# Optimization experiments

Measured on AMD Instinct MI355X. Metric: run time of the kernel, lower is better.

## Reference

```python
import jax, jax.numpy as jnp
import numpy as np

TOP_K = 2

def setup_inputs() -> dict:
    key = jax.random.key(0)
    k1, k2, k3, k4 = jax.random.split(key, 4)
    N, D, E = 16384, 2048, 8
    inputs = jax.random.normal(k1, (N, D), dtype=jnp.float32)
    gate_w = jax.random.normal(k2, (D, E), dtype=jnp.float32) * 0.02
    expert_w = jax.random.normal(k3, (E, D, D), dtype=jnp.float32) * 0.02
    expert_b = jax.random.normal(k4, (E, D), dtype=jnp.float32) * 0.02
    return {"inputs": inputs, "gate_w": gate_w, "expert_w": expert_w, "expert_b": expert_b}

def reference(inputs, gate_w, expert_w, expert_b):
    # gate_logits: [N, E]
    gate_logits = inputs @ gate_w
    # top-k routing: weights/selected_experts are [N, k]
    topk_vals, topk_idx = jax.lax.top_k(gate_logits, TOP_K)
    # softmax over the k selected logits (fp32, matching F.softmax(..., dtype=float))
    weights = jax.nn.softmax(topk_vals.astype(jnp.float32), axis=1).astype(inputs.dtype)
    E = expert_w.shape[0]
    # combine_weights[n, e] = sum_k weights[n, k] * [topk_idx[n, k] == e]
    one_hot = jax.nn.one_hot(topk_idx, E, dtype=weights.dtype)  # [N, k, E]
    combine = jnp.einsum('nk,nke->ne', weights, one_hot)        # [N, E]
    # dense per-expert compute, masked by combine weights (same math as
    # the gather-matmul-scatter loop: unselected experts get weight 0)
    expert_out = jnp.einsum('nd,edh->neh', inputs, expert_w) + expert_b[None]  # [N, E, D]
    return jnp.einsum('ne,ned->nd', combine, expert_out)
```

## Files before the change

kernel.cpp:

```cpp
#include <hip/hip_runtime.h>
#include <stdint.h>

#define N_TOK 16384
#define DIM   2048
#define NEXP  8

#define NTILES 136
#define NSLOTS 36864

typedef __bf16 bf16x8 __attribute__((ext_vector_type(8)));
typedef float  f32x4  __attribute__((ext_vector_type(4)));

__device__ __forceinline__ unsigned short f2bf(float f) {
    union { float f; uint32_t u; } v; v.f = f;
    uint32_t u = v.u;
    u += 0x7fffu + ((u >> 16) & 1u);
    return (unsigned short)(u >> 16);
}

__global__ __launch_bounds__(256) void wconv_kernel(
    const float* __restrict__ W, unsigned short* __restrict__ Wt)
{
    __shared__ float tile[64][65];
    int e  = blockIdx.z;
    int kt = blockIdx.y * 64, nt = blockIdx.x * 64;
    int r4 = threadIdx.x >> 4;
    int c4 = threadIdx.x & 15;
    const float* src = W + ((size_t)e * DIM + kt) * DIM + nt;
#pragma unroll
    for (int i = 0; i < 4; ++i) {
        int r = i * 16 + r4;
        float4 v = *(const float4*)(src + (size_t)r * DIM + c4 * 4);
        tile[r][c4 * 4 + 0] = v.x; tile[r][c4 * 4 + 1] = v.y;
        tile[r][c4 * 4 + 2] = v.z; tile[r][c4 * 4 + 3] = v.w;
    }
    __syncthreads();
    unsigned short* dst = Wt + ((size_t)e * DIM + nt) * DIM + kt;
#pragma unroll
    for (int i = 0; i < 4; ++i) {
        int n = i * 16 + r4;
        ushort4 h;
        h.x = f2bf(tile[c4 * 4 + 0][n]);
        h.y = f2bf(tile[c4 * 4 + 1][n]);
        h.z = f2bf(tile[c4 * 4 + 2][n]);
        h.w = f2bf(tile[c4 * 4 + 3][n]);
        *(ushort4*)(dst + (size_t)n * DIM + c4 * 4) = h;
    }
}

__global__ __launch_bounds__(256) void gate_kernel(
    const float* __restrict__ X, const float* __restrict__ GW,
    unsigned short* __restrict__ Abf, int* __restrict__ tokE,
    float* __restrict__ tokW)
{
    int wave = threadIdx.x >> 6, lane = threadIdx.x & 63;
    int t = blockIdx.x * 4 + wave;
    const float4* xrow = (const float4*)(X + (size_t)t * DIM);
    float acc[NEXP];
#pragma unroll
    for (int e = 0; e < NEXP; ++e) acc[e] = 0.f;
#pragma unroll
    for (int i = 0; i < 8; ++i) {
        int d4 = i * 64 + lane;
        float4 x = xrow[d4];
        ushort4 h;
        h.x = f2bf(x.x); h.y = f2bf(x.y); h.z = f2bf(x.z); h.w = f2bf(x.w);
        *(ushort4*)(Abf + (size_t)t * DIM + (size_t)d4 * 4) = h;
        const float* g = GW + (size_t)d4 * 4 * NEXP;
#pragma unroll
        for (int e = 0; e < NEXP; ++e)
            acc[e] += x.x * g[e] + x.y * g[NEXP + e]
                    + x.z * g[2 * NEXP + e] + x.w * g[3 * NEXP + e];
    }
#pragma unroll
    for (int off = 32; off >= 1; off >>= 1)
#pragma unroll
        for (int e = 0; e < NEXP; ++e)
            acc[e] += __shfl_down(acc[e], off, 64);
    if (lane == 0) {
        int i0 = 0;
#pragma unroll
        for (int e = 1; e < NEXP; ++e) if (acc[e] > acc[i0]) i0 = e;
        int i1 = (i0 == 0) ? 1 : 0;
#pragma unroll
        for (int e = 0; e < NEXP; ++e)
            if (e != i0 && acc[e] > acc[i1]) i1 = e;
        float e1 = expf(acc[i1] - acc[i0]);
        float s  = 1.f + e1;
        tokE[2 * t]     = i0;  tokE[2 * t + 1] = i1;
        tokW[2 * t]     = 1.f / s;
        tokW[2 * t + 1] = e1 / s;
    }
}

__global__ __launch_bounds__(256) void count_kernel(
    const int* __restrict__ tokE, int* __restrict__ counts)
{
    __shared__ int lc[NEXP];
    if (threadIdx.x < NEXP) lc[threadIdx.x] = 0;
    __syncthreads();
#pragma unroll
    for (int p = 0; p < 2; ++p) {
        int i = blockIdx.x * 512 + p * 256 + threadIdx.x;
        atomicAdd(&lc[tokE[i]], 1);
    }
    __syncthreads();
    if (threadIdx.x < NEXP) atomicAdd(&counts[threadIdx.x], lc[threadIdx.x]);
}

__global__ void setup_kernel(const int* __restrict__ counts, int* __restrict__ off,
                             int* __restrict__ tile_e, int* __restrict__ tile_s0)
{
    if (threadIdx.x != 0 || blockIdx.x != 0) return;
    int o = 0, ti = 0;
    for (int e = 0; e < NEXP; ++e) {
        off[e] = o;
        int pc = (counts[e] + 255) & ~255;
        for (int m = 0; m < pc; m += 256) { tile_e[ti] = e; tile_s0[ti] = o + m; ++ti; }
        o += pc;
    }
    for (; ti < NTILES; ++ti) tile_e[ti] = -1;
}

__global__ __launch_bounds__(256) void initperm_kernel(
    int* __restrict__ perm, float* __restrict__ pw)
{
    int i = blockIdx.x * 256 + threadIdx.x;
    perm[i] = -1;
    pw[i]   = 0.f;
}

__global__ __launch_bounds__(256) void assign_kernel(
    const int* __restrict__ tokE, const float* __restrict__ tokW,
    const int* __restrict__ off, int* __restrict__ cursors,
    int* __restrict__ perm, float* __restrict__ pw)
{
    __shared__ int lc[NEXP], lb[NEXP];
    if (threadIdx.x < NEXP) lc[threadIdx.x] = 0;
    __syncthreads();
    int mye[2], myr[2];
#pragma unroll
    for (int p = 0; p < 2; ++p) {
        int i = blockIdx.x * 512 + p * 256 + threadIdx.x;
        mye[p] = tokE[i];
        myr[p] = atomicAdd(&lc[mye[p]], 1);
    }
    __syncthreads();
    if (threadIdx.x < NEXP) lb[threadIdx.x] = atomicAdd(&cursors[threadIdx.x], lc[threadIdx.x]);
    __syncthreads();
#pragma unroll
    for (int p = 0; p < 2; ++p) {
        int i = blockIdx.x * 512 + p * 256 + threadIdx.x;
        int slot = off[mye[p]] + lb[mye[p]] + myr[p];
        perm[slot] = i >> 1;
        pw[slot]   = tokW[i];
    }
}

#define GLD16(gptr, lptr) __builtin_amdgcn_global_load_lds( \
    (const __attribute__((address_space(1))) void*)(gptr),  \
    (__attribute__((address_space(3))) void*)(lptr), 16, 0, 0)

#define MOE_LDS_BYTES (4 * 256 * 64 * 2 + 256 * 4 + 256 * 4)

__global__ __launch_bounds__(512, 2) void moe_gemm(
    const unsigned short* __restrict__ A,
    const unsigned short* __restrict__ Bt,
    const float* __restrict__ bias,
    const int* __restrict__ perm, const float* __restrict__ pw,
    const int* __restrict__ tile_e, const int* __restrict__ tile_s0,
    float* __restrict__ out)
{
    extern __shared__ unsigned short lds[];
    unsigned short* AsB = lds;
    unsigned short* BsB = lds + 2 * 256 * 64;
    int*   toks = (int*)(lds + 4 * 256 * 64);
    float* tws  = (float*)(toks + 256);

    int e = tile_e[blockIdx.y];
    if (e < 0) return;
    int s0 = tile_s0[blockIdx.y];
    int n0 = blockIdx.x * 256;

    int tid = threadIdx.x, wave = tid >> 6, lane = tid & 63;

    if (tid < 256) {
        int t = perm[s0 + tid];
        toks[tid] = (t < 0) ? 0 : t;
        tws[tid]  = (t < 0) ? 0.f : pw[s0 + tid];
    }
    __syncthreads();

    int kof = (((lane & 7) ^ (lane >> 3)) * 8);
    const unsigned short* ab[4];
    const unsigned short* bb[4];
#pragma unroll
    for (int r = 0; r < 4; ++r) {
        int row = r * 64 + wave * 8 + (lane >> 3);
        ab[r] = A + (size_t)toks[row] * DIM + kof;
        bb[r] = Bt + ((size_t)e * DIM + n0 + row) * DIM + kof;
    }

    f32x4 acc[8][4] = {};
    int wr = wave >> 2, wc = wave & 3;
    int wm = wr * 128, wn = wc * 64;
    int fr = lane & 15;
    int q  = lane >> 4;
    int rx = fr & 7;

#define STAGE(buf, k0) do {                                              \
    _Pragma("unroll")                                                    \
    for (int r = 0; r < 4; ++r) {                                        \
        int cb = ((buf) * 16384 + (r * 64 + wave * 8) * 64) * 2;         \
        GLD16(ab[r] + (k0), (char*)AsB + cb);                            \
        GLD16(bb[r] + (k0), (char*)BsB + cb);                            \
    } } while (0)

    STAGE(0, 0);
    __syncthreads();

    int cur = 0;
    for (int t = 0; t < DIM / 64; ++t) {
        if (t + 1 < DIM / 64) STAGE(cur ^ 1, (t + 1) * 64);
        const unsigned short* Ab = AsB + cur * 16384;
        const unsigned short* Bb = BsB + cur * 16384;
#pragma unroll
        for (int kk = 0; kk < 64; kk += 32) {
            int p = (((kk >> 3) + q) ^ rx) * 8;
            bf16x8 af[8], bfr[4];
#pragma unroll
            for (int i = 0; i < 8; ++i)
                af[i] = *(const bf16x8*)(Ab + (wm + i * 16 + fr) * 64 + p);
#pragma unroll
            for (int j = 0; j < 4; ++j)
                bfr[j] = *(const bf16x8*)(Bb + (wn + j * 16 + fr) * 64 + p);
#pragma unroll
            for (int i = 0; i < 8; ++i)
#pragma unroll
                for (int j = 0; j < 4; ++j)
                    acc[i][j] = __builtin_amdgcn_mfma_f32_16x16x32_bf16(
                        af[i], bfr[j], acc[i][j], 0, 0, 0);
        }
        __syncthreads();
        cur ^= 1;
    }

    int rq = (lane >> 4) * 4;
    float bv[4];
#pragma unroll
    for (int j = 0; j < 4; ++j)
        bv[j] = bias[e * DIM + n0 + wn + j * 16 + fr];
#pragma unroll
    for (int i = 0; i < 8; ++i) {
#pragma unroll
        for (int r = 0; r < 4; ++r) {
            int mrow = wm + i * 16 + rq + r;
            float w = tws[mrow];
            if (w != 0.f) {
                float* orow = out + (size_t)toks[mrow] * DIM + n0 + wn;
#pragma unroll
                for (int j = 0; j < 4; ++j)
                    atomicAdd(orow + j * 16 + fr, w * (acc[i][j][r] + bv[j]));
            }
        }
    }
#undef STAGE
}

extern "C" void kernel_launch(void* const* d_in, const int* in_sizes, int n_in,
                              void* d_out, int out_size, void* d_ws, size_t ws_size,
                              hipStream_t stream)
{
    const float* X  = (const float*)d_in[0];
    const float* GW = (const float*)d_in[1];
    const float* W  = (const float*)d_in[2];
    const float* Bb = (const float*)d_in[3];
    float* out = (float*)d_out;

    char* ws = (char*)d_ws;
    unsigned short* Abf = (unsigned short*)ws;
    unsigned short* Wt  = (unsigned short*)(ws + 67108864);
    char* ctrl = ws + 134217728;
    int*   counts  = (int*)(ctrl + 0);
    int*   cursors = (int*)(ctrl + 64);
    int*   off     = (int*)(ctrl + 128);
    int*   tile_e  = (int*)(ctrl + 256);
    int*   tile_s0 = (int*)(ctrl + 2048);
    int*   tokE    = (int*)(ctrl + 4096);
    float* tokW    = (float*)(ctrl + 135168);
    int*   perm    = (int*)(ctrl + 266240);
    float* pw      = (float*)(ctrl + 413696);

    static bool attr_set = false;
    if (!attr_set) {
        hipFuncSetAttribute(reinterpret_cast<const void*>(moe_gemm),
                            hipFuncAttributeMaxDynamicSharedMemorySize,
                            MOE_LDS_BYTES);
        attr_set = true;
    }

    hipMemsetAsync(d_out, 0, (size_t)N_TOK * DIM * sizeof(float), stream);
    hipMemsetAsync(ctrl, 0, 128, stream);

    wconv_kernel <<<dim3(32, 32, NEXP), 256, 0, stream>>>(W, Wt);
    gate_kernel  <<<dim3(N_TOK / 4),    256, 0, stream>>>(X, GW, Abf, tokE, tokW);
    count_kernel <<<dim3(64),           256, 0, stream>>>(tokE, counts);
    setup_kernel <<<dim3(1),             64, 0, stream>>>(counts, off, tile_e, tile_s0);
    initperm_kernel<<<dim3(144),        256, 0, stream>>>(perm, pw);
    assign_kernel<<<dim3(64),           256, 0, stream>>>(tokE, tokW, off, cursors, perm, pw);
    moe_gemm     <<<dim3(8, NTILES), 512, MOE_LDS_BYTES, stream>>>(
        Abf, Wt, Bb, perm, pw, tile_e, tile_s0, out);
}
```

Measured before the change: 880.8 us.

## Restructure MoE GEMM mainloop into fine-grained phased pipeline with split-K LDS layout

Replaces the double-buffered 64-wide K loop with a two-stage, two-half-K (32-wide) LDS layout. Global-to-LDS loads are interleaved phase by phase with MFMA groups, using explicit vmcnt waits, s_barrier, sched_barrier and s_setprio. The aim is to hide load latency behind MFMA work and cut LDS bank conflicts with a new row layout in place of the XOR swizzle. The trade-off is more barriers per K step, fragile hand-tuned wait counts, and wrapped prefetch addresses that load redundant data on the last iterations.

```diff
diff --git a/kernel.cpp b/kernel.cpp
--- a/kernel.cpp
+++ b/kernel.cpp
@@ -161,7 +161,7 @@
     (const __attribute__((address_space(1))) void*)(gptr),  \
     (__attribute__((address_space(3))) void*)(lptr), 16, 0, 0)
 
-#define MOE_LDS_BYTES (4 * 256 * 64 * 2 + 256 * 4 + 256 * 4)
+#define MOE_LDS_BYTES (131072 + 1024 + 1024)
 
 __global__ __launch_bounds__(512, 2) void moe_gemm(
     const unsigned short* __restrict__ A,
@@ -172,10 +172,8 @@
     float* __restrict__ out)
 {
     extern __shared__ unsigned short lds[];
-    unsigned short* AsB = lds;
-    unsigned short* BsB = lds + 2 * 256 * 64;
-    int*   toks = (int*)(lds + 4 * 256 * 64);
-    float* tws  = (float*)(toks + 256);
+    int*   toks = (int*)((char*)lds + 131072);
+    float* tws  = (float*)((char*)lds + 132096);
 
     int e = tile_e[blockIdx.y];
     if (e < 0) return;
@@ -191,58 +189,81 @@
     }
     __syncthreads();
 
-    int kof = (((lane & 7) ^ (lane >> 3)) * 8);
-    const unsigned short* ab[4];
-    const unsigned short* bb[4];
-#pragma unroll
-    for (int r = 0; r < 4; ++r) {
-        int row = r * 64 + wave * 8 + (lane >> 3);
-        ab[r] = A + (size_t)toks[row] * DIM + kof;
-        bb[r] = Bt + ((size_t)e * DIM + n0 + row) * DIM + kof;
-    }
+    int srow = tid & 255, sc = tid >> 8;
+    const unsigned short* pA = A + (size_t)toks[srow] * DIM + sc * 8;
+    const unsigned short* pB = Bt + ((size_t)e * DIM + n0 + srow) * DIM + sc * 8;
+    int wofs = wave * 1024;
+
+#define STAGE_A(s, kh, kofs) do {                                        \
+    int ko_ = (kofs) & (DIM - 1);         \
+    int lb_ = (((s) * 2 + (kh)) << 14) + wofs;                           \
+    GLD16(pA + ko_, (char*)lds + lb_);                                   \
+    GLD16(pA + ko_ + 16, (char*)lds + lb_ + 8192); } while (0)
+#define STAGE_B(s, kh, kofs) do {                                        \
+    int ko_ = (kofs) & (DIM - 1);                                        \
+    int lb_ = 65536 + (((s) * 2 + (kh)) << 14) + wofs;                   \
+    GLD16(pB + ko_, (char*)lds + lb_);                                   \
+    GLD16(pB + ko_ + 16, (char*)lds + lb_ + 8192); } while (0)
 
     f32x4 acc[8][4] = {};
     int wr = wave >> 2, wc = wave & 3;
     int wm = wr * 128, wn = wc * 64;
     int fr = lane & 15;
     int q  = lane >> 4;
-    int rx = fr & 7;
-
-#define STAGE(buf, k0) do {                                              \
-    _Pragma("unroll")                                                    \
-    for (int r = 0; r < 4; ++r) {                                        \
-        int cb = ((buf) * 16384 + (r * 64 + wave * 8) * 64) * 2;         \
-        GLD16(ab[r] + (k0), (char*)AsB + cb);                            \
-        GLD16(bb[r] + (k0), (char*)BsB + cb);                            \
-    } } while (0)
-
-    STAGE(0, 0);
-    __syncthreads();
-
-    int cur = 0;
-    for (int t = 0; t < DIM / 64; ++t) {
-        if (t + 1 < DIM / 64) STAGE(cur ^ 1, (t + 1) * 64);
-        const unsigned short* Ab = AsB + cur * 16384;
-        const unsigned short* Bb = BsB + cur * 16384;
-#pragma unroll
-        for (int kk = 0; kk < 64; kk += 32) {
-            int p = (((kk >> 3) + q) ^ rx) * 8;
-            bf16x8 af[8], bfr[4];
-#pragma unroll
-            for (int i = 0; i < 8; ++i)
-                af[i] = *(const bf16x8*)(Ab + (wm + i * 16 + fr) * 64 + p);
-#pragma unroll
-            for (int j = 0; j < 4; ++j)
-                bfr[j] = *(const bf16x8*)(Bb + (wn + j * 16 + fr) * 64 + p);
-#pragma unroll
-            for (int i = 0; i < 8; ++i)
-#pragma unroll
-                for (int j = 0; j < 4; ++j)
-                    acc[i][j] = __builtin_amdgcn_mfma_f32_16x16x32_bf16(
-                        af[i], bfr[j], acc[i][j], 0, 0, 0);
-        }
-        __syncthreads();
-        cur ^= 1;
+
+    const char* LA = (const char*)lds;
+    const char* LB = (const char*)lds + 65536;
+    int aro = (q << 12) + ((wm + fr) << 4);
+    int bro = (q << 12) + ((wn + fr) << 4);
+
+#define M4(ii, AF)                                                              \
+    acc[ii][0] = __builtin_amdgcn_mfma_f32_16x16x32_bf16(AF, bfr0, acc[ii][0], 0, 0, 0); \
+    acc[ii][1] = __builtin_amdgcn_mfma_f32_16x16x32_bf16(AF, bfr1, acc[ii][1], 0, 0, 0); \
+    acc[ii][2] = __builtin_amdgcn_mfma_f32_16x16x32_bf16(AF, bfr2, acc[ii][2], 0, 0, 0); \
+    acc[ii][3] = __builtin_amdgcn_mfma_f32_16x16x32_bf16(AF, bfr3, acc[ii][3], 0, 0, 0);
+
+#define PHASE(s, kh, ih, LOADB, STG, W) do {                             \
+    asm volatile("" ::: "memory");        \
+    __builtin_amdgcn_sched_barrier(0);                    \
+    int blk_ = (((s) * 2 + (kh)) << 14);                                 \
+    bf16x8 af0 = *(const bf16x8*)(LA + blk_ + aro + ((ih) + 0) * 256);   \
+    bf16x8 af1 = *(const bf16x8*)(LA + blk_ + aro + ((ih) + 1) * 256);   \
+    bf16x8 af2 = *(const bf16x8*)(LA + blk_ + aro + ((ih) + 2) * 256);   \
+    bf16x8 af3 = *(const bf16x8*)(LA + blk_ + aro + ((ih) + 3) * 256);   \
+    if (LOADB) {                                                         \
+        bfr0 = *(const bf16x8*)(LB + blk_ + bro + 0 * 256);              \
+        bfr1 = *(const bf16x8*)(LB + blk_ + bro + 1 * 256);              \
+        bfr2 = *(const bf16x8*)(LB + blk_ + bro + 2 * 256);              \
+        bfr3 = *(const bf16x8*)(LB + blk_ + bro + 3 * 256);              \
+    }                                                                    \
+    STG;                                                                 \
+    if (W) asm volatile("s_waitcnt vmcnt(6)" ::: "memory");              \
+    __builtin_amdgcn_s_barrier();                                        \
+    __builtin_amdgcn_s_setprio(1);                                       \
+    M4((ih) + 0, af0); M4((ih) + 1, af1);                                \
+    M4((ih) + 2, af2); M4((ih) + 3, af3);                                \
+    __builtin_amdgcn_s_setprio(0);                                       \
+    __builtin_amdgcn_s_barrier();                                        \
+} while (0)
+
+    STAGE_B(0, 0, 0);  STAGE_A(0, 0, 0);
+    STAGE_B(0, 1, 32); STAGE_A(0, 1, 32);
+    STAGE_B(1, 0, 64); STAGE_A(1, 0, 64);
+    STAGE_B(1, 1, 96);
+    asm volatile("s_waitcnt vmcnt(6)" ::: "memory");
+    __builtin_amdgcn_s_barrier();
+
+    bf16x8 bfr0, bfr1, bfr2, bfr3;
+#pragma unroll 1
+    for (int kb = 0; kb < DIM; kb += 128) {
+        PHASE(0, 0, 0, 1, STAGE_A(1, 1, kb + 96),  0);
+        PHASE(0, 0, 4, 0, STAGE_B(0, 0, kb + 128), 0);
+        PHASE(0, 1, 0, 1, STAGE_A(0, 0, kb + 128), 0);
+        PHASE(0, 1, 4, 0, STAGE_B(0, 1, kb + 160), 1);
+        PHASE(1, 0, 0, 1, STAGE_A(0, 1, kb + 160), 0);
+        PHASE(1, 0, 4, 0, STAGE_B(1, 0, kb + 192), 0);
+        PHASE(1, 1, 0, 1, STAGE_A(1, 0, kb + 192), 0);
+        PHASE(1, 1, 4, 0, STAGE_B(1, 1, kb + 224), 1);
     }
 
     int rq = (lane >> 4) * 4;
@@ -264,7 +285,10 @@
             }
         }
     }
-#undef STAGE
+#undef PHASE
+#undef M4
+#undef STAGE_A
+#undef STAGE_B
 }
 
 extern "C" void kernel_launch(void* const* d_in, const int* in_sizes, int n_in,
```

Result: slower. 1.024 ms (+16.3%).
